# Kernel tuning notes

Measured on AMD Instinct MI355X. Metric: run time of the kernel, lower is better.

Reference implementation:

```python
import jax, jax.numpy as jnp
import numpy as np

N_HEADS = 12


def gconv1x1(x, w, b, groups):
    # x: [B, C, T, S]; w: [O, C//groups] (1x1 kernel squeezed); b: [O]
    B, C, T, S = x.shape
    O, I = w.shape
    xr = x.reshape(B, groups, C // groups, T, S)
    wr = w.reshape(groups, O // groups, I)
    y = jnp.einsum('bgits,goi->bgots', xr, wr).reshape(B, O, T, S)
    return y + b[None, :, None, None]


def setup_inputs() -> dict:
    key = jax.random.key(0)
    ks = jax.random.split(key, 16)
    B, T, E = 2, 512, 768
    H = N_HEADS
    s = 0.02
    inp = {
        'x': jax.random.normal(ks[0], (B, T, E), jnp.float32),
        # fc_q / fc_k / fc_v (torch Linear: y = x @ W.T + b)
        'wq': jax.random.normal(ks[1], (E, E), jnp.float32) * s,
        'bq': jax.random.normal(ks[2], (E,), jnp.float32) * s,
        'wk': jax.random.normal(ks[3], (E, E), jnp.float32) * s,
        'bk': jax.random.normal(ks[4], (E,), jnp.float32) * s,
        'wv': jax.random.normal(ks[5], (E, E), jnp.float32) * s,
        'bv': jax.random.normal(ks[6], (E,), jnp.float32) * s,
        # ConvolutionOp: all 1x1 grouped convs, groups=12
        # conv_inner_subspace_1: in=144 -> out=96  (w: [96, 12])
        'w1': jax.random.normal(ks[7], (8 * H, H), jnp.float32) * s,
        'b1': jax.random.normal(ks[8], (8 * H,), jnp.float32) * s,
        # conv_inner_subspace_2: in=96 -> out=12   (w: [12, 8])
        'w2': jax.random.normal(ks[9], (H, 8), jnp.float32) * s,
        'b2': jax.random.normal(ks[10], (H,), jnp.float32) * s,
        # conv_cross_subspace_1: in=12 -> out=48   (w: [48, 1])
        'w3': jax.random.normal(ks[11], (4 * H, 1), jnp.float32) * s,
        'b3': jax.random.normal(ks[12], (4 * H,), jnp.float32) * s,
        # conv_cross_subspace_2: in=48 -> out=12   (w: [12, 4])
        'w4': jax.random.normal(ks[13], (H, 4), jnp.float32) * s,
        'b4': jax.random.normal(ks[14], (H,), jnp.float32) * s,
    }
    return inp


def reference(x, wq, bq, wk, bk, wv, bv, w1, b1, w2, b2, w3, b3, w4, b4):
    B, T, E = x.shape
    H = N_HEADS
    hd = E // H
    scale = E ** 0.5  # note: sqrt(embed_dim), not sqrt(head_dim)

    def heads(y):  # [B,T,E] -> [H,B,T,hd]
        return y.reshape(B, T, H, hd).transpose(2, 0, 1, 3)

    q = heads(x @ wq.T + bq)
    k = heads(x @ wk.T + bk)
    v = heads(x @ wv.T + bv)

    # all head-pair QK^T: channel index = q_head * H + k_head (matches torch stack order)
    attn = jnp.einsum('qbld,kbtd->qkblt', q, k) / scale          # [H,H,B,T,T]
    attn = attn.transpose(2, 0, 1, 3, 4).reshape(B, H * H, T, T)  # [B,144,T,T]

    # talking-heads style grouped 1x1 conv mixing
    a = jax.nn.relu(gconv1x1(attn, w1, b1, H))   # [B,96,T,T]
    a = gconv1x1(a, w2, b2, H)                    # [B,12,T,T]
    a = jax.nn.relu(gconv1x1(a, w3, b3, H))      # [B,48,T,T]
    a = gconv1x1(a, w4, b4, H)                    # [B,12,T,T]

    # weighted V sum; rearrange 'head b t d -> b t (head d)'
    ctx = jnp.einsum('bhlt,hbtd->blhd', a, v).reshape(B, T, E)
    return ctx
```

## Files before the change

kernel.cpp:

```cpp
#include <hip/hip_runtime.h>

#define DEVINL __device__ __forceinline__

constexpr int E    = 768;
constexpr int TSEQ = 512;
constexpr int NH   = 12;
constexpr int HD   = 64;
constexpr float RSCALE = 0.036084391824351615f;

typedef short bf16x8 __attribute__((ext_vector_type(8)));
typedef float floatx4 __attribute__((ext_vector_type(4)));

DEVINL short f2bf(float x) {
    union { float f; unsigned u; } v; v.f = x;
    unsigned r = v.u + 0x7FFFu + ((v.u >> 16) & 1u);
    return (short)(r >> 16);
}
DEVINL float bf2f(short s) {
    union { unsigned u; float f; } v;
    v.u = ((unsigned)(unsigned short)s) << 16;
    return v.f;
}

__global__ __launch_bounds__(256) void convert_kernel(
    const float* __restrict__ x,  const float* __restrict__ wq,
    const float* __restrict__ wk, const float* __restrict__ wv,
    short* __restrict__ xb, short* __restrict__ wqb,
    short* __restrict__ wkb, short* __restrict__ wvb)
{
    const int g = blockIdx.x * 256 + threadIdx.x;
    const float* src; short* dst; int off;
    if (g < 98304)       { src = x;  dst = xb;  off = g * 8; }
    else if (g < 172032) { src = wq; dst = wqb; off = (g - 98304) * 8; }
    else if (g < 245760) { src = wk; dst = wkb; off = (g - 172032) * 8; }
    else                 { src = wv; dst = wvb; off = (g - 245760) * 8; }
    float4 f0 = *(const float4*)&src[off];
    float4 f1 = *(const float4*)&src[off + 4];
    bf16x8 o;
    o[0] = f2bf(f0.x); o[1] = f2bf(f0.y); o[2] = f2bf(f0.z); o[3] = f2bf(f0.w);
    o[4] = f2bf(f1.x); o[5] = f2bf(f1.y); o[6] = f2bf(f1.z); o[7] = f2bf(f1.w);
    *(bf16x8*)&dst[off] = o;
}

__global__ __launch_bounds__(256) void qkv_mfma(
    const short* __restrict__ xb,
    const short* __restrict__ wqb, const float* __restrict__ bq,
    const short* __restrict__ wkb, const float* __restrict__ bk,
    const short* __restrict__ wvb, const float* __restrict__ bv,
    short* __restrict__ Qo, short* __restrict__ Ko, short* __restrict__ Vo)
{
    const short* W; const float* bias; short* outp;
    if (blockIdx.z == 0)      { W = wqb; bias = bq; outp = Qo; }
    else if (blockIdx.z == 1) { W = wkb; bias = bk; outp = Ko; }
    else                      { W = wvb; bias = bv; outp = Vo; }

    __shared__ short As[64 * 72];
    __shared__ short Bs[64 * 72];

    const int m0   = blockIdx.x * 64;
    const int n0   = blockIdx.y * 64;
    const int tid  = threadIdx.x;
    const int wvi  = tid >> 6;
    const int lane = tid & 63;
    const int col  = lane & 15;
    const int quad = lane >> 4;

    const int r0 = tid >> 3,   kc0 = tid & 7;
    const int r1 = r0 + 32;

    floatx4 acc[4];
    #pragma unroll
    for (int i = 0; i < 4; i++) acc[i] = (floatx4){0.f, 0.f, 0.f, 0.f};

    for (int k0 = 0; k0 < E; k0 += 64) {
        bf16x8 a0 = *(const bf16x8*)&xb[(size_t)(m0 + r0) * E + k0 + kc0 * 8];
        bf16x8 a1 = *(const bf16x8*)&xb[(size_t)(m0 + r1) * E + k0 + kc0 * 8];
        bf16x8 b0 = *(const bf16x8*)&W [(size_t)(n0 + r0) * E + k0 + kc0 * 8];
        bf16x8 b1 = *(const bf16x8*)&W [(size_t)(n0 + r1) * E + k0 + kc0 * 8];
        __syncthreads();
        *(bf16x8*)&As[r0 * 72 + kc0 * 8] = a0;
        *(bf16x8*)&As[r1 * 72 + kc0 * 8] = a1;
        *(bf16x8*)&Bs[r0 * 72 + kc0 * 8] = b0;
        *(bf16x8*)&Bs[r1 * 72 + kc0 * 8] = b1;
        __syncthreads();
        #pragma unroll
        for (int k32 = 0; k32 < 2; k32++) {
            bf16x8 bf = *(const bf16x8*)&Bs[(wvi*16 + col) * 72 + k32*32 + quad*8];
            #pragma unroll
            for (int ms = 0; ms < 4; ms++) {
                bf16x8 af = *(const bf16x8*)&As[(ms*16 + col) * 72 + k32*32 + quad*8];
                acc[ms] = __builtin_amdgcn_mfma_f32_16x16x32_bf16(af, bf, acc[ms], 0, 0, 0);
            }
        }
    }

    const float bn = bias[n0 + wvi*16 + col];
    const int h = blockIdx.y;
    #pragma unroll
    for (int ms = 0; ms < 4; ms++) {
        #pragma unroll
        for (int r = 0; r < 4; r++) {
            int m = m0 + ms*16 + quad*4 + r;
            int bb = m >> 9, l = m & 511;
            outp[(((size_t)(bb*NH + h)) * TSEQ + l) * HD + wvi*16 + col] =
                f2bf(acc[ms][r] + bn);
        }
    }
}

__global__ __launch_bounds__(256) void kmix_kernel(
    const short* __restrict__ K,
    const float* __restrict__ w1,
    short* __restrict__ Kp)
{
    const int g  = blockIdx.x * 256 + threadIdx.x;
    const int d8 = g & 7;
    const int t  = (g >> 3) & 511;
    const int o  = (g >> 12) & 7;
    const int bh = g >> 15;
    const int h  = bh % NH;
    const int b  = bh / NH;

    float acc[8] = {};
    #pragma unroll
    for (int i = 0; i < 12; i++) {
        float w = w1[(h*8 + o)*12 + i] * RSCALE;
        bf16x8 kv = *(const bf16x8*)&K[(((size_t)(b*NH + i) * TSEQ) + t) * HD + d8*8];
        #pragma unroll
        for (int j = 0; j < 8; j++)
            acc[j] = fmaf(w, bf2f(kv[j]), acc[j]);
    }
    bf16x8 outv;
    #pragma unroll
    for (int j = 0; j < 8; j++) outv[j] = f2bf(acc[j]);
    *(bf16x8*)&Kp[(size_t)g * 8] = outv;
}

DEVINL float mlp_eval(const float s[8],
                      const float b1r[8], const float w2r[8], float b2r,
                      const float w3r[4], const float b3r[4],
                      const float w4r[4], float b4r)
{
    float z2 = b2r;
    #pragma unroll
    for (int o = 0; o < 8; o++) {
        float z1 = fmaxf(s[o] + b1r[o], 0.0f);
        z2 = fmaf(z1, w2r[o], z2);
    }
    float r = b4r;
    #pragma unroll
    for (int j = 0; j < 4; j++) {
        float z3 = fmaxf(fmaf(z2, w3r[j], b3r[j]), 0.0f);
        r = fmaf(z3, w4r[j], r);
    }
    return r;
}

DEVINL int vrow(int r) { return r*40 + (r >> 3)*8; }

__global__ __launch_bounds__(256, 3) void attn_mfma(
    const short* __restrict__ Qg,
    const short* __restrict__ Kg,
    const short* __restrict__ Vg,
    const float* __restrict__ b1, const float* __restrict__ w2,
    const float* __restrict__ b2, const float* __restrict__ w3,
    const float* __restrict__ b3, const float* __restrict__ w4,
    const float* __restrict__ b4,
    float* __restrict__ Pout)
{
    __shared__ short Ks[256 * 72];
    __shared__ short Vt[2624];
    __shared__ short As[2624];

    const int hw   = blockIdx.x;
    const int xcd  = hw & 7;
    const int slot = hw >> 3;
    const int bh   = xcd * 3 + (slot >> 5);
    const int inner= slot & 31;
    const int lt   = inner >> 2;
    const int qtr  = inner & 3;
    const int blk  = (bh * 8 + lt) * 4 + qtr;

    const int h   = bh % NH;
    const int l0  = lt * 64;
    const int tb  = qtr * 128;

    const int tid  = threadIdx.x;
    const int wv   = tid >> 6;
    const int lane = tid & 63;
    const int col  = lane & 15;
    const int quad = lane >> 4;
    const int wl   = wv >> 1;
    const int wt   = wv & 1;

    float b1r[8], w2r[8], w3r[4], b3r[4], w4r[4];
    #pragma unroll
    for (int o = 0; o < 8; o++) { b1r[o] = b1[h*8+o]; w2r[o] = w2[h*8+o]; }
    #pragma unroll
    for (int j = 0; j < 4; j++) { w3r[j] = w3[h*4+j]; b3r[j] = b3[h*4+j]; w4r[j] = w4[h*4+j]; }
    const float b2r = b2[h];
    const float b4r = b4[h];

    bf16x8 qa[2][2];
    {
        const short* qb = Qg + ((size_t)bh * TSEQ + l0 + wl*32 + col) * HD;
        qa[0][0] = *(const bf16x8*)&qb[quad*8];
        qa[0][1] = *(const bf16x8*)&qb[32 + quad*8];
        qa[1][0] = *(const bf16x8*)&qb[16*HD + quad*8];
        qa[1][1] = *(const bf16x8*)&qb[16*HD + 32 + quad*8];
    }

    floatx4 accO[4];
    #pragma unroll
    for (int d16 = 0; d16 < 4; d16++) accO[d16] = (floatx4){0.f, 0.f, 0.f, 0.f};

    const short* kbase = Kg + (size_t)bh * 8 * TSEQ * HD;
    const short* vbase = Vg + (size_t)bh * TSEQ * HD;

    const int tl = tid >> 3;
    const int dc = tid & 7;

    for (int it = 0; it < 4; it++) {
        const int t0 = tb + it * 32;

        bf16x8 ktmp[8];
        #pragma unroll
        for (int o = 0; o < 8; o++)
            ktmp[o] = *(const bf16x8*)&kbase[((size_t)o * TSEQ + t0 + tl) * HD + dc*8];
        bf16x8 vtmp = *(const bf16x8*)&vbase[(size_t)(t0 + tl) * HD + dc*8];

        __syncthreads();

        #pragma unroll
        for (int o = 0; o < 8; o++)
            *(bf16x8*)&Ks[(o*32 + tl)*72 + dc*8] = ktmp[o];
        #pragma unroll
        for (int j = 0; j < 8; j++)
            Vt[vrow(dc*8 + j) + tl] = vtmp[j];

        __syncthreads();

        floatx4 accS[8][2];
        #pragma unroll
        for (int o = 0; o < 8; o++) {
            accS[o][0] = (floatx4){0.f, 0.f, 0.f, 0.f};
            accS[o][1] = (floatx4){0.f, 0.f, 0.f, 0.f};
        }
        #pragma unroll
        for (int k32 = 0; k32 < 2; k32++) {
            #pragma unroll
            for (int o = 0; o < 8; o++) {
                bf16x8 bf = *(const bf16x8*)&Ks[(o*32 + wt*16 + col)*72 + k32*32 + quad*8];
                accS[o][0] = __builtin_amdgcn_mfma_f32_16x16x32_bf16(qa[0][k32], bf, accS[o][0], 0, 0, 0);
                accS[o][1] = __builtin_amdgcn_mfma_f32_16x16x32_bf16(qa[1][k32], bf, accS[o][1], 0, 0, 0);
            }
        }

        #pragma unroll
        for (int li = 0; li < 2; li++) {
            #pragma unroll
            for (int r = 0; r < 4; r++) {
                float s[8];
                #pragma unroll
                for (int o = 0; o < 8; o++) s[o] = accS[o][li][r];
                float a = mlp_eval(s, b1r, w2r, b2r, w3r, b3r, w4r, b4r);
                As[vrow(wl*32 + li*16 + quad*4 + r) + wt*16 + col] = f2bf(a);
            }
        }
        __syncthreads();

        bf16x8 af = *(const bf16x8*)&As[vrow(wv*16 + col) + quad*8];
        #pragma unroll
        for (int d16 = 0; d16 < 4; d16++) {
            bf16x8 vf = *(const bf16x8*)&Vt[vrow(d16*16 + col) + quad*8];
            accO[d16] = __builtin_amdgcn_mfma_f32_16x16x32_bf16(af, vf, accO[d16], 0, 0, 0);
        }
    }

    float* pb = Pout + (size_t)blk * 64 * 64;
    #pragma unroll
    for (int d16 = 0; d16 < 4; d16++)
        #pragma unroll
        for (int r = 0; r < 4; r++)
            pb[(wv*16 + quad*4 + r) * 64 + d16*16 + col] = accO[d16][r];
}

__global__ __launch_bounds__(256) void reduce_kernel(
    const float* __restrict__ P, float* __restrict__ out)
{
    const int gi  = blockIdx.x * 256 + threadIdx.x;
    const int d4  = gi & 15;
    const int r   = (gi >> 4) & 63;
    const int grp = gi >> 10;
    const int lt  = grp & 7;
    const int bh  = grp >> 3;
    const int h   = bh % NH;
    const int b   = bh / NH;

    const float* p0 = P + (size_t)grp * 4 * 4096 + r * 64 + d4 * 4;
    float4 s0 = *(const float4*)&p0[0];
    float4 s1 = *(const float4*)&p0[4096];
    float4 s2 = *(const float4*)&p0[8192];
    float4 s3 = *(const float4*)&p0[12288];
    float4 s;
    s.x = (s0.x + s1.x) + (s2.x + s3.x);
    s.y = (s0.y + s1.y) + (s2.y + s3.y);
    s.z = (s0.z + s1.z) + (s2.z + s3.z);
    s.w = (s0.w + s1.w) + (s2.w + s3.w);
    *(float4*)&out[((size_t)(b*TSEQ + lt*64 + r)) * E + h*64 + d4*4] = s;
}

extern "C" void kernel_launch(void* const* d_in, const int* in_sizes, int n_in,
                              void* d_out, int out_size, void* d_ws, size_t ws_size,
                              hipStream_t stream) {
    const float* x  = (const float*)d_in[0];
    const float* wq = (const float*)d_in[1];
    const float* bq = (const float*)d_in[2];
    const float* wk = (const float*)d_in[3];
    const float* bk = (const float*)d_in[4];
    const float* wv = (const float*)d_in[5];
    const float* bv = (const float*)d_in[6];
    const float* w1 = (const float*)d_in[7];
    const float* b1 = (const float*)d_in[8];
    const float* w2 = (const float*)d_in[9];
    const float* b2 = (const float*)d_in[10];
    const float* w3 = (const float*)d_in[11];
    const float* b3 = (const float*)d_in[12];
    const float* w4 = (const float*)d_in[13];
    const float* b4 = (const float*)d_in[14];
    float* out = (float*)d_out;

    short* Qb = (short*)d_ws;
    short* Kb = Qb + 786432;
    short* Vb = Kb + 786432;
    short* Kp = Vb + 786432;
    float* P  = (float*)(Kp + 6291456);
    short* xb  = (short*)P;
    short* wqb = xb + 786432;
    short* wkb = wqb + 589824;
    short* wvb = wkb + 589824;

    convert_kernel<<<1248, 256, 0, stream>>>(x, wq, wk, wv, xb, wqb, wkb, wvb);
    qkv_mfma<<<dim3(16, 12, 3), 256, 0, stream>>>(xb, wqb, bq, wkb, bk, wvb, bv, Qb, Kb, Vb);
    kmix_kernel<<<3072, 256, 0, stream>>>(Kb, w1, Kp);
    attn_mfma<<<768, 256, 0, stream>>>(Qb, Kp, Vb, b1, w2, b2, w3, b3, w4, b4, P);
    reduce_kernel<<<768, 256, 0, stream>>>(P, out);
}
```

Measured before the change: 132.2 us.

## Fuse split-T reduction into attention via atomics and prefetch QKV GEMM tiles

Removes the separate reduce kernel and partial-sum buffer. The attention kernel now atomically adds its partial context directly into the zeroed output, with a memset added up front. The QKV GEMM also register-prefetches the next K tile before computing the current one, to overlap global loads with MFMA work. The atomics add contention across four blocks per output and make float summation order nondeterministic.

```diff
diff --git a/kernel.cpp b/kernel.cpp
--- a/kernel.cpp
+++ b/kernel.cpp
@@ -72,17 +72,26 @@
     #pragma unroll
     for (int i = 0; i < 4; i++) acc[i] = (floatx4){0.f, 0.f, 0.f, 0.f};
 
+    bf16x8 a0 = *(const bf16x8*)&xb[(size_t)(m0 + r0) * E + kc0 * 8];
+    bf16x8 a1 = *(const bf16x8*)&xb[(size_t)(m0 + r1) * E + kc0 * 8];
+    bf16x8 b0 = *(const bf16x8*)&W [(size_t)(n0 + r0) * E + kc0 * 8];
+    bf16x8 b1 = *(const bf16x8*)&W [(size_t)(n0 + r1) * E + kc0 * 8];
+
     for (int k0 = 0; k0 < E; k0 += 64) {
-        bf16x8 a0 = *(const bf16x8*)&xb[(size_t)(m0 + r0) * E + k0 + kc0 * 8];
-        bf16x8 a1 = *(const bf16x8*)&xb[(size_t)(m0 + r1) * E + k0 + kc0 * 8];
-        bf16x8 b0 = *(const bf16x8*)&W [(size_t)(n0 + r0) * E + k0 + kc0 * 8];
-        bf16x8 b1 = *(const bf16x8*)&W [(size_t)(n0 + r1) * E + k0 + kc0 * 8];
         __syncthreads();
         *(bf16x8*)&As[r0 * 72 + kc0 * 8] = a0;
         *(bf16x8*)&As[r1 * 72 + kc0 * 8] = a1;
         *(bf16x8*)&Bs[r0 * 72 + kc0 * 8] = b0;
         *(bf16x8*)&Bs[r1 * 72 + kc0 * 8] = b1;
         __syncthreads();
+
+        if (k0 + 64 < E) {
+            a0 = *(const bf16x8*)&xb[(size_t)(m0 + r0) * E + k0 + 64 + kc0 * 8];
+            a1 = *(const bf16x8*)&xb[(size_t)(m0 + r1) * E + k0 + 64 + kc0 * 8];
+            b0 = *(const bf16x8*)&W [(size_t)(n0 + r0) * E + k0 + 64 + kc0 * 8];
+            b1 = *(const bf16x8*)&W [(size_t)(n0 + r1) * E + k0 + 64 + kc0 * 8];
+        }
+
         #pragma unroll
         for (int k32 = 0; k32 < 2; k32++) {
             bf16x8 bf = *(const bf16x8*)&Bs[(wvi*16 + col) * 72 + k32*32 + quad*8];
@@ -166,7 +175,7 @@
     const float* __restrict__ b2, const float* __restrict__ w3,
     const float* __restrict__ b3, const float* __restrict__ w4,
     const float* __restrict__ b4,
-    float* __restrict__ Pout)
+    float* __restrict__ out)
 {
     __shared__ short Ks[256 * 72];
     __shared__ short Vt[2624];
@@ -179,9 +188,9 @@
     const int inner= slot & 31;
     const int lt   = inner >> 2;
     const int qtr  = inner & 3;
-    const int blk  = (bh * 8 + lt) * 4 + qtr;
 
     const int h   = bh % NH;
+    const int b   = bh / NH;
     const int l0  = lt * 64;
     const int tb  = qtr * 128;
 
@@ -277,37 +286,12 @@
         }
     }
 
-    float* pb = Pout + (size_t)blk * 64 * 64;
-    #pragma unroll
-    for (int d16 = 0; d16 < 4; d16++)
-        #pragma unroll
-        for (int r = 0; r < 4; r++)
-            pb[(wv*16 + quad*4 + r) * 64 + d16*16 + col] = accO[d16][r];
-}
-
-__global__ __launch_bounds__(256) void reduce_kernel(
-    const float* __restrict__ P, float* __restrict__ out)
-{
-    const int gi  = blockIdx.x * 256 + threadIdx.x;
-    const int d4  = gi & 15;
-    const int r   = (gi >> 4) & 63;
-    const int grp = gi >> 10;
-    const int lt  = grp & 7;
-    const int bh  = grp >> 3;
-    const int h   = bh % NH;
-    const int b   = bh / NH;
-
-    const float* p0 = P + (size_t)grp * 4 * 4096 + r * 64 + d4 * 4;
-    float4 s0 = *(const float4*)&p0[0];
-    float4 s1 = *(const float4*)&p0[4096];
-    float4 s2 = *(const float4*)&p0[8192];
-    float4 s3 = *(const float4*)&p0[12288];
-    float4 s;
-    s.x = (s0.x + s1.x) + (s2.x + s3.x);
-    s.y = (s0.y + s1.y) + (s2.y + s3.y);
-    s.z = (s0.z + s1.z) + (s2.z + s3.z);
-    s.w = (s0.w + s1.w) + (s2.w + s3.w);
-    *(float4*)&out[((size_t)(b*TSEQ + lt*64 + r)) * E + h*64 + d4*4] = s;
+    float* ob = out + ((size_t)(b*TSEQ + l0 + wv*16 + quad*4)) * E + h*HD + col;
+    #pragma unroll
+    for (int r = 0; r < 4; r++)
+        #pragma unroll
+        for (int d16 = 0; d16 < 4; d16++)
+            atomicAdd(&ob[(size_t)r * E + d16*16], accO[d16][r]);
 }
 
 extern "C" void kernel_launch(void* const* d_in, const int* in_sizes, int n_in,
@@ -330,19 +314,18 @@
     const float* b4 = (const float*)d_in[14];
     float* out = (float*)d_out;
 
-    short* Qb = (short*)d_ws;
-    short* Kb = Qb + 786432;
-    short* Vb = Kb + 786432;
-    short* Kp = Vb + 786432;
-    float* P  = (float*)(Kp + 6291456);
-    short* xb  = (short*)P;
+    short* Qb  = (short*)d_ws;
+    short* Kb  = Qb + 786432;
+    short* Vb  = Kb + 786432;
+    short* Kp  = Vb + 786432;
+    short* xb  = Kp + 6291456;
     short* wqb = xb + 786432;
     short* wkb = wqb + 589824;
     short* wvb = wkb + 589824;
 
+    hipMemsetAsync(out, 0, (size_t)out_size * sizeof(float), stream);
     convert_kernel<<<1248, 256, 0, stream>>>(x, wq, wk, wv, xb, wqb, wkb, wvb);
     qkv_mfma<<<dim3(16, 12, 3), 256, 0, stream>>>(xb, wqb, bq, wkb, bk, wvb, bv, Qb, Kb, Vb);
     kmix_kernel<<<3072, 256, 0, stream>>>(Kb, w1, Kp);
-    attn_mfma<<<768, 256, 0, stream>>>(Qb, Kp, Vb, b1, w2, b2, w3, b3, w4, b4, P);
-    reduce_kernel<<<768, 256, 0, stream>>>(P, out);
-}
+    attn_mfma<<<768, 256, 0, stream>>>(Qb, Kp, Vb, b1, w2, b2, w3, b3, w4, b4, out);
+}
```

Result: slower. 141.1 us (+6.7%).

## Load K fragments directly from global, preload V tiles, stream MLP over channel pairs

Applied to the files above, without the earlier changes.

Drops the shared-memory staging of the eight K' channel tiles: each wave now reads its MFMA B fragments straight from global memory. All four V tiles are transposed into LDS once up front, which removes per-iteration V staging and one barrier. The first MLP layer is accumulated over channel pairs so only two channels of S accumulators are live at a time, and launch bounds are raised to four blocks per CU. The cost is that K fragment reads now rely on the cache rather than coalesced LDS staging, and the per-block LDS footprint changes.

```diff
diff --git a/kernel.cpp b/kernel.cpp
--- a/kernel.cpp
+++ b/kernel.cpp
@@ -136,29 +136,9 @@
     *(bf16x8*)&Kp[(size_t)g * 8] = outv;
 }
 
-DEVINL float mlp_eval(const float s[8],
-                      const float b1r[8], const float w2r[8], float b2r,
-                      const float w3r[4], const float b3r[4],
-                      const float w4r[4], float b4r)
-{
-    float z2 = b2r;
-    #pragma unroll
-    for (int o = 0; o < 8; o++) {
-        float z1 = fmaxf(s[o] + b1r[o], 0.0f);
-        z2 = fmaf(z1, w2r[o], z2);
-    }
-    float r = b4r;
-    #pragma unroll
-    for (int j = 0; j < 4; j++) {
-        float z3 = fmaxf(fmaf(z2, w3r[j], b3r[j]), 0.0f);
-        r = fmaf(z3, w4r[j], r);
-    }
-    return r;
-}
-
 DEVINL int vrow(int r) { return r*40 + (r >> 3)*8; }
 
-__global__ __launch_bounds__(256, 3) void attn_mfma(
+__global__ __launch_bounds__(256, 4) void attn_mfma(
     const short* __restrict__ Qg,
     const short* __restrict__ Kg,
     const short* __restrict__ Vg,
@@ -168,8 +148,7 @@
     const float* __restrict__ b4,
     float* __restrict__ Pout)
 {
-    __shared__ short Ks[256 * 72];
-    __shared__ short Vt[2624];
+    __shared__ short Vt[4 * 2624];
     __shared__ short As[2624];
 
     const int hw   = blockIdx.x;
@@ -210,69 +189,86 @@
         qa[1][1] = *(const bf16x8*)&qb[16*HD + 32 + quad*8];
     }
 
-    floatx4 accO[4];
-    #pragma unroll
-    for (int d16 = 0; d16 < 4; d16++) accO[d16] = (floatx4){0.f, 0.f, 0.f, 0.f};
-
     const short* kbase = Kg + (size_t)bh * 8 * TSEQ * HD;
     const short* vbase = Vg + (size_t)bh * TSEQ * HD;
 
-    const int tl = tid >> 3;
-    const int dc = tid & 7;
+    {
+        const int tl = tid >> 3;
+        const int dc = tid & 7;
+        #pragma unroll
+        for (int tq = 0; tq < 4; tq++) {
+            bf16x8 vtmp = *(const bf16x8*)&vbase[(size_t)(tb + tq*32 + tl) * HD + dc*8];
+            #pragma unroll
+            for (int j = 0; j < 8; j++)
+                Vt[tq*2624 + vrow(dc*8 + j) + tl] = vtmp[j];
+        }
+    }
+    __syncthreads();
+
+    floatx4 accO[4];
+    #pragma unroll
+    for (int d16 = 0; d16 < 4; d16++) accO[d16] = (floatx4){0.f, 0.f, 0.f, 0.f};
+
+    const int tg = tb + wt*16 + col;
 
     for (int it = 0; it < 4; it++) {
-        const int t0 = tb + it * 32;
-
-        bf16x8 ktmp[8];
-        #pragma unroll
-        for (int o = 0; o < 8; o++)
-            ktmp[o] = *(const bf16x8*)&kbase[((size_t)o * TSEQ + t0 + tl) * HD + dc*8];
-        bf16x8 vtmp = *(const bf16x8*)&vbase[(size_t)(t0 + tl) * HD + dc*8];
+        float z2v[2][4];
+        #pragma unroll
+        for (int li = 0; li < 2; li++)
+            #pragma unroll
+            for (int r = 0; r < 4; r++) z2v[li][r] = b2r;
+
+        #pragma unroll
+        for (int oh = 0; oh < 8; oh += 2) {
+            floatx4 accS[2][2];
+            #pragma unroll
+            for (int o2 = 0; o2 < 2; o2++) {
+                accS[o2][0] = (floatx4){0.f, 0.f, 0.f, 0.f};
+                accS[o2][1] = (floatx4){0.f, 0.f, 0.f, 0.f};
+            }
+            #pragma unroll
+            for (int k32 = 0; k32 < 2; k32++) {
+                #pragma unroll
+                for (int o2 = 0; o2 < 2; o2++) {
+                    bf16x8 bfr = *(const bf16x8*)&kbase[
+                        ((size_t)(oh + o2) * TSEQ + it*32 + tg) * HD + k32*32 + quad*8];
+                    accS[o2][0] = __builtin_amdgcn_mfma_f32_16x16x32_bf16(qa[0][k32], bfr, accS[o2][0], 0, 0, 0);
+                    accS[o2][1] = __builtin_amdgcn_mfma_f32_16x16x32_bf16(qa[1][k32], bfr, accS[o2][1], 0, 0, 0);
+                }
+            }
+            #pragma unroll
+            for (int o2 = 0; o2 < 2; o2++) {
+                const float b1o = b1r[oh+o2], w2o = w2r[oh+o2];
+                #pragma unroll
+                for (int li = 0; li < 2; li++)
+                    #pragma unroll
+                    for (int r = 0; r < 4; r++)
+                        z2v[li][r] = fmaf(fmaxf(accS[o2][li][r] + b1o, 0.0f), w2o, z2v[li][r]);
+            }
+        }
 
         __syncthreads();
 
         #pragma unroll
-        for (int o = 0; o < 8; o++)
-            *(bf16x8*)&Ks[(o*32 + tl)*72 + dc*8] = ktmp[o];
-        #pragma unroll
-        for (int j = 0; j < 8; j++)
-            Vt[vrow(dc*8 + j) + tl] = vtmp[j];
-
+        for (int li = 0; li < 2; li++) {
+            #pragma unroll
+            for (int r = 0; r < 4; r++) {
+                float z2 = z2v[li][r];
+                float a = b4r;
+                #pragma unroll
+                for (int j = 0; j < 4; j++) {
+                    float z3 = fmaxf(fmaf(z2, w3r[j], b3r[j]), 0.0f);
+                    a = fmaf(z3, w4r[j], a);
+                }
+                As[vrow(wl*32 + li*16 + quad*4 + r) + wt*16 + col] = f2bf(a);
+            }
+        }
         __syncthreads();
 
-        floatx4 accS[8][2];
-        #pragma unroll
-        for (int o = 0; o < 8; o++) {
-            accS[o][0] = (floatx4){0.f, 0.f, 0.f, 0.f};
-            accS[o][1] = (floatx4){0.f, 0.f, 0.f, 0.f};
-        }
-        #pragma unroll
-        for (int k32 = 0; k32 < 2; k32++) {
-            #pragma unroll
-            for (int o = 0; o < 8; o++) {
-                bf16x8 bf = *(const bf16x8*)&Ks[(o*32 + wt*16 + col)*72 + k32*32 + quad*8];
-                accS[o][0] = __builtin_amdgcn_mfma_f32_16x16x32_bf16(qa[0][k32], bf, accS[o][0], 0, 0, 0);
-                accS[o][1] = __builtin_amdgcn_mfma_f32_16x16x32_bf16(qa[1][k32], bf, accS[o][1], 0, 0, 0);
-            }
-        }
-
-        #pragma unroll
-        for (int li = 0; li < 2; li++) {
-            #pragma unroll
-            for (int r = 0; r < 4; r++) {
-                float s[8];
-                #pragma unroll
-                for (int o = 0; o < 8; o++) s[o] = accS[o][li][r];
-                float a = mlp_eval(s, b1r, w2r, b2r, w3r, b3r, w4r, b4r);
-                As[vrow(wl*32 + li*16 + quad*4 + r) + wt*16 + col] = f2bf(a);
-            }
-        }
-        __syncthreads();
-
         bf16x8 af = *(const bf16x8*)&As[vrow(wv*16 + col) + quad*8];
         #pragma unroll
         for (int d16 = 0; d16 < 4; d16++) {
-            bf16x8 vf = *(const bf16x8*)&Vt[vrow(d16*16 + col) + quad*8];
+            bf16x8 vf = *(const bf16x8*)&Vt[it*2624 + vrow(d16*16 + col) + quad*8];
             accO[d16] = __builtin_amdgcn_mfma_f32_16x16x32_bf16(af, vf, accO[d16], 0, 0, 0);
         }
     }
```

New measurement: 146.5 us. 10.8% more time.
